# Performance work log

Measured on AMD Instinct MI355X. Metric: run time of the kernel, lower is better.

## Reference

```python
import math
import jax, jax.numpy as jnp
import numpy as np

B = 128          # graphs per batch
N = 1024         # nodes per graph
E = 1048576      # total edges (avg degree 8)
F_IN = 64
NHID = 64
NCLS = 10
RATIO = 0.8


def setup_inputs() -> dict:
    key = jax.random.key(0)
    ks = jax.random.split(key, 24)
    x = jax.random.normal(ks[0], (B * N, F_IN), jnp.float32)
    # intra-graph random edges: graph id per edge, local src/dst
    epg = E // B
    gid = jnp.repeat(jnp.arange(B, dtype=jnp.int32), epg)
    src = gid * N + jax.random.randint(ks[1], (E,), 0, N, jnp.int32)
    dst = gid * N + jax.random.randint(ks[2], (E,), 0, N, jnp.int32)
    def lin(k, fi, fo):
        s = 1.0 / np.sqrt(fi)
        return jax.random.uniform(k, (fi, fo), jnp.float32, -s, s)
    p = {
        'W1': lin(ks[3], F_IN, NHID), 'b1': jnp.zeros((NHID,), jnp.float32),
        'Wp1': lin(ks[4], NHID, 1), 'bp1': jnp.zeros((1,), jnp.float32),
        'W2': lin(ks[5], NHID, NHID), 'b2': jnp.zeros((NHID,), jnp.float32),
        'Wp2': lin(ks[6], NHID, 1), 'bp2': jnp.zeros((1,), jnp.float32),
        'W3': lin(ks[7], NHID, NHID), 'b3': jnp.zeros((NHID,), jnp.float32),
        'Wp3': lin(ks[8], NHID, 1), 'bp3': jnp.zeros((1,), jnp.float32),
        'L1w': lin(ks[9], 2 * NHID, NHID), 'L1b': jnp.zeros((NHID,), jnp.float32),
        'L2w': lin(ks[10], NHID, NHID // 2), 'L2b': jnp.zeros((NHID // 2,), jnp.float32),
        'L3w': lin(ks[11], NHID // 2, NCLS), 'L3b': jnp.zeros((NCLS,), jnp.float32),
    }
    return dict(x=x, edge_src=src, edge_dst=dst, **p)


def gcn_conv(x, W, b, src, dst, emask, n):
    # PyG GCNConv: add self loops, symmetric deg normalization
    xw = x @ W
    ew = emask.astype(x.dtype)
    deg = jax.ops.segment_sum(ew, dst, num_segments=n) + 1.0  # +1 self loop
    dis = jax.lax.rsqrt(deg)
    norm = dis[src] * dis[dst] * ew
    agg = jax.ops.segment_sum(xw[src] * norm[:, None], dst, num_segments=n)
    agg = agg + xw * (dis * dis)[:, None]  # self-loop message
    return agg + b


def sag_pool(x, Wp, bp, src, dst, emask, n_cur):
    n_tot = B * n_cur
    k = int(math.ceil(RATIO * n_cur))
    score = gcn_conv(x, Wp, bp, src, dst, emask, n_tot)[:, 0]
    _, idx = jax.lax.top_k(score.reshape(B, n_cur), k)
    perm = (idx + (jnp.arange(B, dtype=jnp.int32) * n_cur)[:, None]).reshape(-1)
    xn = x[perm] * jnp.tanh(score[perm])[:, None]
    new_idx = jnp.full((n_tot,), -1, jnp.int32).at[perm].set(
        jnp.arange(B * k, dtype=jnp.int32))
    ns, nd = new_idx[src], new_idx[dst]
    valid = emask & (ns >= 0) & (nd >= 0)
    return xn, jnp.where(valid, ns, 0), jnp.where(valid, nd, 0), valid, k


def readout(x, k):
    xr = x.reshape(B, k, NHID)
    return jnp.concatenate([xr.max(axis=1), xr.mean(axis=1)], axis=1)


def reference(x, edge_src, edge_dst, W1, b1, Wp1, bp1, W2, b2, Wp2, bp2,
              W3, b3, Wp3, bp3, L1w, L1b, L2w, L2b, L3w, L3b):
    src = edge_src.astype(jnp.int32)
    dst = edge_dst.astype(jnp.int32)
    emask = jnp.ones((E,), bool)
    n = N
    h = jax.nn.relu(gcn_conv(x, W1, b1, src, dst, emask, B * n))
    h, src, dst, emask, n = sag_pool(h, Wp1, bp1, src, dst, emask, n)
    r1 = readout(h, n)
    h = jax.nn.relu(gcn_conv(h, W2, b2, src, dst, emask, B * n))
    h, src, dst, emask, n = sag_pool(h, Wp2, bp2, src, dst, emask, n)
    r2 = readout(h, n)
    h = jax.nn.relu(gcn_conv(h, W3, b3, src, dst, emask, B * n))
    h, src, dst, emask, n = sag_pool(h, Wp3, bp3, src, dst, emask, n)
    r3 = readout(h, n)
    z = r1 + r2 + r3
    z = jax.nn.relu(z @ L1w + L1b)          # dropout is identity in eval
    z = jax.nn.relu(z @ L2w + L2b)
    return jax.nn.log_softmax(z @ L3w + L3b, axis=-1)
```

## Files before the change

### kernel.cpp

```cpp
#include <hip/hip_runtime.h>
#include <math.h>

constexpr int B_  = 128;
constexpr int N_  = 1024;
constexpr int E_  = 1048576;
constexpr int BN_ = B_ * N_;
constexpr int EPG = E_ / B_;
constexpr int NSEG = 16;

typedef short v8s __attribute__((ext_vector_type(8)));
typedef float v4f __attribute__((ext_vector_type(4)));

__device__ __forceinline__ unsigned bf16_rne(unsigned u) {
    return (u + 0x7FFFu + ((u >> 16) & 1u)) >> 16;
}

__global__ __launch_bounds__(1024) void k_csr(
        const int* __restrict__ src, const int* __restrict__ dst,
        int* __restrict__ srt, int* __restrict__ rowptr,
        float* __restrict__ dis, int n) {
    __shared__ int cnt[1024];
    __shared__ int cur[1024];
    __shared__ int wsum[17];
    int g = blockIdx.x, tid = threadIdx.x;
    int base = g * n;
    const int eb = g * EPG;

    for (int i = tid; i < n; i += 1024) cnt[i] = 0;
    __syncthreads();
    for (int t = tid; t < EPG; t += 1024) {
        int s = src[eb + t];
        if (s >= 0) atomicAdd(&cnt[dst[eb + t] - base], 1);
    }
    __syncthreads();

    int c = (tid < n) ? cnt[tid] : 0;
    int v = c;
    int lane = tid & 63, wv = tid >> 6;
    #pragma unroll
    for (int off = 1; off < 64; off <<= 1) {
        int t = __shfl_up(v, off, 64);
        if (lane >= off) v += t;
    }
    if (lane == 63) wsum[wv] = v;
    __syncthreads();
    if (tid == 0) {
        int run = 0;
        #pragma unroll
        for (int i = 0; i < 16; ++i) { int t = wsum[i]; wsum[i] = run; run += t; }
        wsum[16] = run;
    }
    __syncthreads();
    int excl = v - c + wsum[wv];
    if (tid < n) {
        cur[tid] = excl;
        rowptr[g * (n + 1) + tid] = excl;
        dis[base + tid] = rsqrtf((float)c + 1.0f);
    }
    if (tid == 0) rowptr[g * (n + 1) + n] = wsum[16];
    __syncthreads();

    for (int t = tid; t < EPG; t += 1024) {
        int s = src[eb + t];
        if (s < 0) continue;
        int pos = atomicAdd(&cur[dst[eb + t] - base], 1);
        srt[eb + pos] = s - base;
    }
}

__global__ __launch_bounds__(1024) void k_wprep3(
        const float* __restrict__ W0, const float* __restrict__ W1,
        const float* __restrict__ W2, unsigned short* __restrict__ wfall) {
    const float* W = (blockIdx.x == 0) ? W0 : (blockIdx.x == 1) ? W1 : W2;
    unsigned short* wf = wfall + (size_t)blockIdx.x * 8192;
    int t = threadIdx.x;
    int l  = t & 63;
    int kk = (t >> 6) & 1;
    int c  = (t >> 7) & 3;
    int p  = (t >> 9) & 1;
    int col = c * 16 + (l & 15);
    int kbase = kk * 32 + (l >> 4) * 8;
    unsigned short o[8];
    #pragma unroll
    for (int j = 0; j < 8; ++j) {
        float w = W[(kbase + j) * 64 + col];
        unsigned u  = __float_as_uint(w);
        unsigned hi = bf16_rne(u);
        if (p == 0) o[j] = (unsigned short)hi;
        else {
            float lo = w - __uint_as_float(hi << 16);
            o[j] = (unsigned short)bf16_rne(__float_as_uint(lo));
        }
    }
    uint4 v;
    v.x = o[0] | ((unsigned)o[1] << 16);
    v.y = o[2] | ((unsigned)o[3] << 16);
    v.z = o[4] | ((unsigned)o[5] << 16);
    v.w = o[6] | ((unsigned)o[7] << 16);
    *reinterpret_cast<uint4*>(wf + (size_t)t * 8) = v;
}

__global__ __launch_bounds__(256) void k_xw_mfma(
        const float* __restrict__ h, const unsigned short* __restrict__ wf,
        const float* __restrict__ dis, float* __restrict__ xwq, int rows) {
    __shared__ float hs[128][68];
    __shared__ float sdis[128];
    int tid = threadIdx.x;
    int r0 = blockIdx.x * 128;

    for (int i = tid; i < 128 * 16; i += 256) {
        int row = i >> 4, s = i & 15;
        float4 v = *reinterpret_cast<const float4*>(h + (size_t)(r0 + row) * 64 + s * 4);
        *reinterpret_cast<float4*>(&hs[row][s * 4]) = v;
    }
    if (tid < 128) sdis[tid] = dis[r0 + tid];

    int lane = tid & 63;
    v8s wh[4][2], wl[4][2];
    #pragma unroll
    for (int c = 0; c < 4; ++c) {
        #pragma unroll
        for (int kk = 0; kk < 2; ++kk) {
            wh[c][kk] = *reinterpret_cast<const v8s*>(wf + (((size_t)((0*4 + c)*2 + kk))*64 + lane)*8);
            wl[c][kk] = *reinterpret_cast<const v8s*>(wf + (((size_t)((1*4 + c)*2 + kk))*64 + lane)*8);
        }
    }
    __syncthreads();

    int wave = tid >> 6;
    int m = lane & 15, b = lane >> 4;
    #pragma unroll
    for (int t = 0; t < 2; ++t) {
        int lr0 = (wave * 2 + t) * 16;
        float f[16];
        *reinterpret_cast<float4*>(f)      = *reinterpret_cast<const float4*>(&hs[lr0 + m][b * 8]);
        *reinterpret_cast<float4*>(f + 4)  = *reinterpret_cast<const float4*>(&hs[lr0 + m][b * 8 + 4]);
        *reinterpret_cast<float4*>(f + 8)  = *reinterpret_cast<const float4*>(&hs[lr0 + m][32 + b * 8]);
        *reinterpret_cast<float4*>(f + 12) = *reinterpret_cast<const float4*>(&hs[lr0 + m][32 + b * 8 + 4]);
        v8s ah[2], al[2];
        #pragma unroll
        for (int ch = 0; ch < 2; ++ch) {
            #pragma unroll
            for (int j = 0; j < 8; ++j) {
                float x = f[ch * 8 + j];
                unsigned u  = __float_as_uint(x);
                unsigned hi = bf16_rne(u);
                float lo = x - __uint_as_float(hi << 16);
                ah[ch][j] = (short)hi;
                al[ch][j] = (short)bf16_rne(__float_as_uint(lo));
            }
        }
        float dv[4];
        #pragma unroll
        for (int reg = 0; reg < 4; ++reg) dv[reg] = sdis[lr0 + b * 4 + reg];

        #pragma unroll
        for (int c = 0; c < 4; ++c) {
            v4f acc = {0.f, 0.f, 0.f, 0.f};
            acc = __builtin_amdgcn_mfma_f32_16x16x32_bf16(ah[0], wh[c][0], acc, 0, 0, 0);
            acc = __builtin_amdgcn_mfma_f32_16x16x32_bf16(ah[1], wh[c][1], acc, 0, 0, 0);
            acc = __builtin_amdgcn_mfma_f32_16x16x32_bf16(al[0], wh[c][0], acc, 0, 0, 0);
            acc = __builtin_amdgcn_mfma_f32_16x16x32_bf16(al[1], wh[c][1], acc, 0, 0, 0);
            acc = __builtin_amdgcn_mfma_f32_16x16x32_bf16(ah[0], wl[c][0], acc, 0, 0, 0);
            acc = __builtin_amdgcn_mfma_f32_16x16x32_bf16(ah[1], wl[c][1], acc, 0, 0, 0);
            acc = __builtin_amdgcn_mfma_f32_16x16x32_bf16(al[0], wl[c][0], acc, 0, 0, 0);
            acc = __builtin_amdgcn_mfma_f32_16x16x32_bf16(al[1], wl[c][1], acc, 0, 0, 0);
            #pragma unroll
            for (int reg = 0; reg < 4; ++reg) {
                int grow = r0 + lr0 + b * 4 + reg;
                xwq[((size_t)c * rows + grow) * 16 + m] = acc[reg] * dv[reg];
            }
        }
    }
}

__global__ __launch_bounds__(1024) void k_agg_csr(
        const int* __restrict__ srt, const int* __restrict__ rowptr,
        const float* __restrict__ dis, const float* __restrict__ xwq,
        const float* __restrict__ bias, float* __restrict__ hout,
        int n, int rows) {
    extern __shared__ float lds[];
    float* xs  = lds;
    int* lsrt  = (int*)(lds + n * 20);
    int* lrp   = lsrt + EPG;
    int g = blockIdx.x >> 2, q = blockIdx.x & 3;
    int foff = q * 16;
    int tid  = threadIdx.x;
    int base = g * n;
    const float* plane = xwq + ((size_t)q * rows + base) * 16;

    for (int i = tid; i < n * 4; i += 1024) {
        int row = i >> 2, sub = i & 3;
        float4 v = *reinterpret_cast<const float4*>(plane + row * 16 + sub * 4);
        *reinterpret_cast<float4*>(xs + row * 20 + sub * 4) = v;
    }
    for (int i = tid; i <= n; i += 1024) lrp[i] = rowptr[g * (n + 1) + i];
    __syncthreads();
    int total = lrp[n];
    const int* gsrt = srt + g * EPG;
    for (int i = tid; i < total; i += 1024) lsrt[i] = gsrt[i];
    __syncthreads();

    int sub = tid & 3;
    float4 b = *reinterpret_cast<const float4*>(bias + foff + sub * 4);
    for (int row = tid >> 2; row < n; row += 256) {
        int s0 = lrp[row], s1 = lrp[row + 1];
        float4 acc = *reinterpret_cast<const float4*>(xs + row * 20 + sub * 4);
        for (int j = s0; j < s1; ++j) {
            int s = lsrt[j];
            const float4 v = *reinterpret_cast<const float4*>(xs + s * 20 + sub * 4);
            acc.x += v.x; acc.y += v.y; acc.z += v.z; acc.w += v.w;
        }
        float dsc = dis[base + row];
        float4 o;
        o.x = fmaxf(fmaf(dsc, acc.x, b.x), 0.0f);
        o.y = fmaxf(fmaf(dsc, acc.y, b.y), 0.0f);
        o.z = fmaxf(fmaf(dsc, acc.z, b.z), 0.0f);
        o.w = fmaxf(fmaf(dsc, acc.w, b.w), 0.0f);
        *reinterpret_cast<float4*>(hout + (size_t)(base + row) * 64 + foff + sub * 4) = o;
    }
}

__global__ void k_score(const float* __restrict__ h, const float* __restrict__ Wp,
                        const float* __restrict__ dis, float* __restrict__ sxws, int rows) {
    __shared__ float wp[64];
    if (threadIdx.x < 64) wp[threadIdx.x] = Wp[threadIdx.x];
    __syncthreads();
    int r = blockIdx.x * blockDim.x + threadIdx.x;
    if (r >= rows) return;
    const float4* hr = reinterpret_cast<const float4*>(h + (size_t)r * 64);
    float acc = 0.0f;
    #pragma unroll
    for (int kk = 0; kk < 16; ++kk) {
        float4 v = hr[kk];
        acc += v.x * wp[4*kk] + v.y * wp[4*kk+1] + v.z * wp[4*kk+2] + v.w * wp[4*kk+3];
    }
    sxws[r] = acc * dis[r];
}

__global__ __launch_bounds__(1024) void k_score_csr(
        const int* __restrict__ srt, const int* __restrict__ rowptr,
        const float* __restrict__ dis, const float* __restrict__ sxws,
        float* __restrict__ sagg, int n) {
    __shared__ float xs[1024];
    __shared__ int lrp[1025];
    __shared__ int lsrt[EPG];
    int g = blockIdx.x, tid = threadIdx.x;
    int base = g * n;
    for (int i = tid; i < n; i += 1024) xs[i] = sxws[base + i];
    for (int i = tid; i <= n; i += 1024) lrp[i] = rowptr[g * (n + 1) + i];
    __syncthreads();
    int total = lrp[n];
    for (int i = tid; i < total; i += 1024) lsrt[i] = srt[g * EPG + i];
    __syncthreads();
    if (tid < n) {
        float acc = xs[tid];
        int s1 = lrp[tid + 1];
        for (int j = lrp[tid]; j < s1; ++j) acc += xs[lsrt[j]];
        sagg[base + tid] = dis[base + tid] * acc;
    }
}

__global__ __launch_bounds__(512) void k_topk(
        const float* __restrict__ sagg, const float* __restrict__ bp,
        int n, int k, int* __restrict__ perm, int* __restrict__ new_idx) {
    __shared__ unsigned long long keys[1024];
    int g = blockIdx.x, tid = threadIdx.x;
    float bp0 = bp[0];
    for (int i = tid; i < 1024; i += 512) {
        unsigned long long kv = 0ull;
        if (i < n) {
            float sc = sagg[g * n + i] + bp0;
            unsigned u  = __float_as_uint(sc);
            unsigned mk = (u & 0x80000000u) ? ~u : (u | 0x80000000u);
            kv = ((unsigned long long)mk << 32) | (unsigned)i;
        }
        keys[i] = kv;
    }
    for (int size = 2; size <= 1024; size <<= 1) {
        for (int stride = size >> 1; stride > 0; stride >>= 1) {
            __syncthreads();
            int p = tid;
            int a  = ((p / stride) * (stride << 1)) + (p & (stride - 1));
            int bx = a + stride;
            bool asc = ((a & size) == 0);
            unsigned long long ka = keys[a], kb = keys[bx];
            bool sw = asc ? (ka > kb) : (ka < kb);
            if (sw) { keys[a] = kb; keys[bx] = ka; }
        }
    }
    __syncthreads();
    for (int j = tid; j < k; j += 512) {
        int pos   = 1023 - j;
        int local = (int)(keys[pos] & 0xFFFFFFFFull);
        int oldg  = g * n + local;
        int newg  = g * k + j;
        perm[newg]    = oldg;
        new_idx[oldg] = newg;
    }
}

__global__ __launch_bounds__(256) void k_gather_part(
        const float* __restrict__ h, const int* __restrict__ perm,
        const float* __restrict__ sagg, const float* __restrict__ bp,
        float* __restrict__ xn, int k, float* __restrict__ pz) {
    int g = blockIdx.x / NSEG, seg = blockIdx.x % NSEG;
    int ck = (k + NSEG - 1) / NSEG;
    int j0 = seg * ck;
    int j1 = min(k, j0 + ck);
    __shared__ float gate[64];
    __shared__ int   lperm[64];
    int tid = threadIdx.x;
    float bp0 = bp[0];
    for (int j = j0 + tid; j < j1; j += 256) {
        int old = perm[g * k + j];
        lperm[j - j0] = old;
        gate[j - j0]  = tanhf(sagg[old] + bp0);
    }
    __syncthreads();
    int lane = tid & 63, w = tid >> 6;
    float mx = -INFINITY, sm = 0.0f;
    for (int j = j0 + w; j < j1; j += 4) {
        int old = lperm[j - j0];
        float v = h[(size_t)old * 64 + lane] * gate[j - j0];
        xn[(size_t)(g * k + j) * 64 + lane] = v;
        mx = fmaxf(mx, v); sm += v;
    }
    __shared__ float smx[4][64], ssm[4][64];
    smx[w][lane] = mx; ssm[w][lane] = sm;
    __syncthreads();
    if (w == 0) {
        #pragma unroll
        for (int i = 1; i < 4; ++i) { mx = fmaxf(mx, smx[i][lane]); sm += ssm[i][lane]; }
        float* p = pz + ((size_t)g * NSEG + seg) * 128;
        p[lane]      = mx;
        p[64 + lane] = sm;
    }
}

__global__ __launch_bounds__(128) void k_combine(const float* __restrict__ pz,
                                                 int k, float* __restrict__ zsum) {
    int g = blockIdx.x, tid = threadIdx.x;
    const float* p = pz + (size_t)g * NSEG * 128;
    if (tid < 64) {
        float mx = -INFINITY;
        #pragma unroll
        for (int s = 0; s < NSEG; ++s) mx = fmaxf(mx, p[s * 128 + tid]);
        zsum[g * 128 + tid] += mx;
    } else {
        float sm = 0.0f;
        int f = tid - 64;
        #pragma unroll
        for (int s = 0; s < NSEG; ++s) sm += p[s * 128 + 64 + f];
        zsum[g * 128 + 64 + f] += sm / (float)k;
    }
}

__global__ void k_remap(const int* __restrict__ src, const int* __restrict__ dst,
                        const int* __restrict__ new_idx,
                        int* __restrict__ src2, int* __restrict__ dst2, int E) {
    int e = blockIdx.x * blockDim.x + threadIdx.x;
    if (e >= E) return;
    int s = src[e];
    int ns = -1, nd = -1;
    if (s >= 0) {
        ns = new_idx[s];
        nd = new_idx[dst[e]];
    }
    bool ok = (ns >= 0) && (nd >= 0);
    src2[e] = ok ? ns : -1;
    dst2[e] = ok ? nd : -1;
}

__global__ void k_mlp(const float* __restrict__ zsum,
                      const float* __restrict__ L1w, const float* __restrict__ L1b,
                      const float* __restrict__ L2w, const float* __restrict__ L2b,
                      const float* __restrict__ L3w, const float* __restrict__ L3b,
                      float* __restrict__ out) {
    __shared__ float z[128], h1[64], h2[32], lg[10], lse;
    int g = blockIdx.x, tid = threadIdx.x;
    z[tid] = zsum[g * 128 + tid];
    __syncthreads();
    if (tid < 64) {
        float acc = L1b[tid];
        for (int i = 0; i < 128; ++i) acc = fmaf(z[i], L1w[i * 64 + tid], acc);
        h1[tid] = fmaxf(acc, 0.0f);
    }
    __syncthreads();
    if (tid < 32) {
        float acc = L2b[tid];
        for (int i = 0; i < 64; ++i) acc = fmaf(h1[i], L2w[i * 32 + tid], acc);
        h2[tid] = fmaxf(acc, 0.0f);
    }
    __syncthreads();
    if (tid < 10) {
        float acc = L3b[tid];
        for (int i = 0; i < 32; ++i) acc = fmaf(h2[i], L3w[i * 10 + tid], acc);
        lg[tid] = acc;
    }
    __syncthreads();
    if (tid == 0) {
        float m = lg[0];
        for (int i = 1; i < 10; ++i) m = fmaxf(m, lg[i]);
        float s = 0.0f;
        for (int i = 0; i < 10; ++i) s += expf(lg[i] - m);
        lse = m + logf(s);
    }
    __syncthreads();
    if (tid < 10) out[g * 10 + tid] = lg[tid] - lse;
}

extern "C" void kernel_launch(void* const* d_in, const int* in_sizes, int n_in,
                              void* d_out, int out_size, void* d_ws, size_t ws_size,
                              hipStream_t stream) {
    const float* x    = (const float*)d_in[0];
    const int*   esrc = (const int*)d_in[1];
    const int*   edst = (const int*)d_in[2];
    const float* W [3] = {(const float*)d_in[3],  (const float*)d_in[7],  (const float*)d_in[11]};
    const float* bb[3] = {(const float*)d_in[4],  (const float*)d_in[8],  (const float*)d_in[12]};
    const float* Wp[3] = {(const float*)d_in[5],  (const float*)d_in[9],  (const float*)d_in[13]};
    const float* bp[3] = {(const float*)d_in[6],  (const float*)d_in[10], (const float*)d_in[14]};
    const float* L1w = (const float*)d_in[15];
    const float* L1b = (const float*)d_in[16];
    const float* L2w = (const float*)d_in[17];
    const float* L2b = (const float*)d_in[18];
    const float* L3w = (const float*)d_in[19];
    const float* L3b = (const float*)d_in[20];
    float* out = (float*)d_out;

    float* fws  = (float*)d_ws;
    float* bufA = fws;
    float* xwq  = bufA + 6717440;
    float* agg  = xwq  + 8388608;
    float* dis  = agg  + 8388608;
    float* sxws = dis  + BN_;
    float* sagg = sxws + BN_;
    float* zsum = sagg + BN_;
    float* pz   = zsum + 128 * 128;
    int*   new_idx = (int*)(pz + B_ * NSEG * 128);
    int*   perm    = new_idx + BN_;
    int*   srcB    = perm + BN_;
    int*   dstB    = srcB + E_;
    int*   srcC    = dstB + E_;
    int*   dstC    = srcC + E_;
    int*   srt     = dstC + E_;
    int*   rowptr  = srt  + E_;
    unsigned short* wfrag = (unsigned short*)(rowptr + B_ * (N_ + 1));

    hipFuncSetAttribute(reinterpret_cast<const void*>(k_agg_csr),
                        hipFuncAttributeMaxDynamicSharedMemorySize,
                        (1024 * 20 + EPG + 1025) * 4);

    hipMemsetAsync(zsum, 0, 128 * 128 * sizeof(float), stream);
    k_wprep3<<<3, 1024, 0, stream>>>(W[0], W[1], W[2], wfrag);

    const int ks_[3] = {820, 656, 525};
    int n = N_;
    const float* h_in = x;
    const int* cs = esrc;
    const int* cd = edst;
    int* nsrc[2] = {srcB, srcC};
    int* ndst[2] = {dstB, dstC};

    const int EB = (E_ + 255) / 256;

    for (int L = 0; L < 3; ++L) {
        int rows  = B_ * n;
        int k     = ks_[L];

        k_csr<<<B_, 1024, 0, stream>>>(cs, cd, srt, rowptr, dis, n);

        k_xw_mfma<<<rows / 128, 256, 0, stream>>>(h_in, wfrag + (size_t)L * 8192, dis, xwq, rows);
        k_agg_csr<<<B_ * 4, 1024, (size_t)(n * 20 + EPG + n + 1) * 4, stream>>>(
            srt, rowptr, dis, xwq, bb[L], agg, n, rows);

        k_score<<<(rows + 255) / 256, 256, 0, stream>>>(agg, Wp[L], dis, sxws, rows);
        k_score_csr<<<B_, 1024, 0, stream>>>(srt, rowptr, dis, sxws, sagg, n);

        if (L < 2) hipMemsetAsync(new_idx, 0xFF, (size_t)rows * sizeof(int), stream);
        k_topk<<<B_, 512, 0, stream>>>(sagg, bp[L], n, k, perm, new_idx);
        k_gather_part<<<B_ * NSEG, 256, 0, stream>>>(agg, perm, sagg, bp[L], bufA, k, pz);
        k_combine<<<B_, 128, 0, stream>>>(pz, k, zsum);
        if (L < 2) k_remap<<<EB, 256, 0, stream>>>(cs, cd, new_idx, nsrc[L], ndst[L], E_);

        h_in = bufA;
        n = k;
        if (L < 2) { cs = nsrc[L]; cd = ndst[L]; }
    }

    k_mlp<<<B_, 128, 0, stream>>>(zsum, L1w, L1b, L2w, L2b, L3w, L3b, out);
}
```

Baseline: 273.6 us.

## Fuse score, top-k, gather and edge remap into cumulative node-index mapping

```diff
diff --git a/kernel.cpp b/kernel.cpp
--- a/kernel.cpp
+++ b/kernel.cpp
@@ -15,22 +15,27 @@
     return (u + 0x7FFFu + ((u >> 16) & 1u)) >> 16;
 }
 
-__global__ __launch_bounds__(1024) void k_csr(
+__global__ __launch_bounds__(1024) void k_csr2(
         const int* __restrict__ src, const int* __restrict__ dst,
+        const int* __restrict__ cum,
         int* __restrict__ srt, int* __restrict__ rowptr,
         float* __restrict__ dis, int n) {
     __shared__ int cnt[1024];
     __shared__ int cur[1024];
+    __shared__ int cums[1024];
     __shared__ int wsum[17];
     int g = blockIdx.x, tid = threadIdx.x;
+    int gb   = g * N_;
     int base = g * n;
     const int eb = g * EPG;
 
-    for (int i = tid; i < n; i += 1024) cnt[i] = 0;
+    cums[tid] = cum ? cum[gb + tid] : tid;
+    cnt[tid] = 0;
     __syncthreads();
     for (int t = tid; t < EPG; t += 1024) {
-        int s = src[eb + t];
-        if (s >= 0) atomicAdd(&cnt[dst[eb + t] - base], 1);
+        int s = cums[src[eb + t] - gb];
+        int d = cums[dst[eb + t] - gb];
+        if ((s | d) >= 0) atomicAdd(&cnt[d], 1);
     }
     __syncthreads();
 
@@ -61,10 +66,11 @@
     __syncthreads();
 
     for (int t = tid; t < EPG; t += 1024) {
-        int s = src[eb + t];
-        if (s < 0) continue;
-        int pos = atomicAdd(&cur[dst[eb + t] - base], 1);
-        srt[eb + pos] = s - base;
+        int s = cums[src[eb + t] - gb];
+        int d = cums[dst[eb + t] - gb];
+        if ((s | d) < 0) continue;
+        int pos = atomicAdd(&cur[d], 1);
+        srt[eb + pos] = s;
     }
 }
 
@@ -101,17 +107,32 @@
 }
 
 __global__ __launch_bounds__(256) void k_xw_mfma(
-        const float* __restrict__ h, const unsigned short* __restrict__ wf,
+        const float* __restrict__ h, const int* __restrict__ perm,
+        const float* __restrict__ ggate, const unsigned short* __restrict__ wf,
         const float* __restrict__ dis, float* __restrict__ xwq, int rows) {
     __shared__ float hs[128][68];
     __shared__ float sdis[128];
+    __shared__ int   lperm[128];
+    __shared__ float lgate[128];
     int tid = threadIdx.x;
     int r0 = blockIdx.x * 128;
 
-    for (int i = tid; i < 128 * 16; i += 256) {
-        int row = i >> 4, s = i & 15;
-        float4 v = *reinterpret_cast<const float4*>(h + (size_t)(r0 + row) * 64 + s * 4);
-        *reinterpret_cast<float4*>(&hs[row][s * 4]) = v;
+    if (perm) {
+        if (tid < 128) { lperm[tid] = perm[r0 + tid]; lgate[tid] = ggate[r0 + tid]; }
+        __syncthreads();
+        for (int i = tid; i < 128 * 16; i += 256) {
+            int row = i >> 4, s = i & 15;
+            float4 v = *reinterpret_cast<const float4*>(h + (size_t)lperm[row] * 64 + s * 4);
+            float gt = lgate[row];
+            v.x *= gt; v.y *= gt; v.z *= gt; v.w *= gt;
+            *reinterpret_cast<float4*>(&hs[row][s * 4]) = v;
+        }
+    } else {
+        for (int i = tid; i < 128 * 16; i += 256) {
+            int row = i >> 4, s = i & 15;
+            float4 v = *reinterpret_cast<const float4*>(h + (size_t)(r0 + row) * 64 + s * 4);
+            *reinterpret_cast<float4*>(&hs[row][s * 4]) = v;
+        }
     }
     if (tid < 128) sdis[tid] = dis[r0 + tid];
 
@@ -177,7 +198,8 @@
 __global__ __launch_bounds__(1024) void k_agg_csr(
         const int* __restrict__ srt, const int* __restrict__ rowptr,
         const float* __restrict__ dis, const float* __restrict__ xwq,
-        const float* __restrict__ bias, float* __restrict__ hout,
+        const float* __restrict__ bias, const float* __restrict__ Wp,
+        float* __restrict__ hout, float* __restrict__ sxwsq,
         int n, int rows) {
     extern __shared__ float lds[];
     float* xs  = lds;
@@ -202,7 +224,8 @@
     __syncthreads();
 
     int sub = tid & 3;
-    float4 b = *reinterpret_cast<const float4*>(bias + foff + sub * 4);
+    float4 b   = *reinterpret_cast<const float4*>(bias + foff + sub * 4);
+    float4 wp4 = *reinterpret_cast<const float4*>(Wp   + foff + sub * 4);
     for (int row = tid >> 2; row < n; row += 256) {
         int s0 = lrp[row], s1 = lrp[row + 1];
         float4 acc = *reinterpret_cast<const float4*>(xs + row * 20 + sub * 4);
@@ -218,92 +241,96 @@
         o.z = fmaxf(fmaf(dsc, acc.z, b.z), 0.0f);
         o.w = fmaxf(fmaf(dsc, acc.w, b.w), 0.0f);
         *reinterpret_cast<float4*>(hout + (size_t)(base + row) * 64 + foff + sub * 4) = o;
-    }
-}
-
-__global__ void k_score(const float* __restrict__ h, const float* __restrict__ Wp,
-                        const float* __restrict__ dis, float* __restrict__ sxws, int rows) {
-    __shared__ float wp[64];
-    if (threadIdx.x < 64) wp[threadIdx.x] = Wp[threadIdx.x];
-    __syncthreads();
-    int r = blockIdx.x * blockDim.x + threadIdx.x;
-    if (r >= rows) return;
-    const float4* hr = reinterpret_cast<const float4*>(h + (size_t)r * 64);
-    float acc = 0.0f;
-    #pragma unroll
-    for (int kk = 0; kk < 16; ++kk) {
-        float4 v = hr[kk];
-        acc += v.x * wp[4*kk] + v.y * wp[4*kk+1] + v.z * wp[4*kk+2] + v.w * wp[4*kk+3];
-    }
-    sxws[r] = acc * dis[r];
-}
-
-__global__ __launch_bounds__(1024) void k_score_csr(
+        float part = o.x * wp4.x + o.y * wp4.y + o.z * wp4.z + o.w * wp4.w;
+        part += __shfl_xor(part, 1, 64);
+        part += __shfl_xor(part, 2, 64);
+        if (sub == 0) sxwsq[(size_t)q * BN_ + base + row] = part;
+    }
+}
+
+__global__ __launch_bounds__(1024) void k_score_topk(
         const int* __restrict__ srt, const int* __restrict__ rowptr,
-        const float* __restrict__ dis, const float* __restrict__ sxws,
-        float* __restrict__ sagg, int n) {
+        const float* __restrict__ dis, const float* __restrict__ sxwsq,
+        const float* __restrict__ bp, int n, int k,
+        int* __restrict__ perm, float* __restrict__ ggate,
+        int* __restrict__ cum, int do_compose) {
     __shared__ float xs[1024];
-    __shared__ int lrp[1025];
-    __shared__ int lsrt[EPG];
+    __shared__ int   lrp[1025];
+    __shared__ int   lsrt[EPG];
+    unsigned long long* keys = (unsigned long long*)lsrt;
+    int* mark = (int*)xs;
     int g = blockIdx.x, tid = threadIdx.x;
     int base = g * n;
-    for (int i = tid; i < n; i += 1024) xs[i] = sxws[base + i];
+    float bp0 = bp[0];
+
+    if (tid < n) {
+        float s0 = sxwsq[0 * (size_t)BN_ + base + tid] + sxwsq[1 * (size_t)BN_ + base + tid]
+                 + sxwsq[2 * (size_t)BN_ + base + tid] + sxwsq[3 * (size_t)BN_ + base + tid];
+        xs[tid] = s0 * dis[base + tid];
+    }
     for (int i = tid; i <= n; i += 1024) lrp[i] = rowptr[g * (n + 1) + i];
     __syncthreads();
     int total = lrp[n];
     for (int i = tid; i < total; i += 1024) lsrt[i] = srt[g * EPG + i];
     __syncthreads();
+
+    float sag = 0.0f;
     if (tid < n) {
         float acc = xs[tid];
         int s1 = lrp[tid + 1];
         for (int j = lrp[tid]; j < s1; ++j) acc += xs[lsrt[j]];
-        sagg[base + tid] = dis[base + tid] * acc;
-    }
-}
-
-__global__ __launch_bounds__(512) void k_topk(
-        const float* __restrict__ sagg, const float* __restrict__ bp,
-        int n, int k, int* __restrict__ perm, int* __restrict__ new_idx) {
-    __shared__ unsigned long long keys[1024];
-    int g = blockIdx.x, tid = threadIdx.x;
-    float bp0 = bp[0];
-    for (int i = tid; i < 1024; i += 512) {
+        sag = dis[base + tid] * acc + bp0;
+    }
+    __syncthreads();
+
+    {
         unsigned long long kv = 0ull;
-        if (i < n) {
-            float sc = sagg[g * n + i] + bp0;
-            unsigned u  = __float_as_uint(sc);
+        if (tid < n) {
+            unsigned u  = __float_as_uint(sag);
             unsigned mk = (u & 0x80000000u) ? ~u : (u | 0x80000000u);
-            kv = ((unsigned long long)mk << 32) | (unsigned)i;
-        }
-        keys[i] = kv;
-    }
+            kv = ((unsigned long long)mk << 32) | (unsigned)tid;
+        }
+        keys[tid] = kv;
+        mark[tid] = -1;
+    }
+
     for (int size = 2; size <= 1024; size <<= 1) {
         for (int stride = size >> 1; stride > 0; stride >>= 1) {
             __syncthreads();
-            int p = tid;
-            int a  = ((p / stride) * (stride << 1)) + (p & (stride - 1));
-            int bx = a + stride;
-            bool asc = ((a & size) == 0);
-            unsigned long long ka = keys[a], kb = keys[bx];
-            bool sw = asc ? (ka > kb) : (ka < kb);
-            if (sw) { keys[a] = kb; keys[bx] = ka; }
-        }
-    }
-    __syncthreads();
-    for (int j = tid; j < k; j += 512) {
-        int pos   = 1023 - j;
-        int local = (int)(keys[pos] & 0xFFFFFFFFull);
-        int oldg  = g * n + local;
-        int newg  = g * k + j;
-        perm[newg]    = oldg;
-        new_idx[oldg] = newg;
-    }
-}
-
-__global__ __launch_bounds__(256) void k_gather_part(
+            if (tid < 512) {
+                int a  = ((tid / stride) * (stride << 1)) + (tid & (stride - 1));
+                int bx = a + stride;
+                bool asc = ((a & size) == 0);
+                unsigned long long ka = keys[a], kb = keys[bx];
+                bool sw = asc ? (ka > kb) : (ka < kb);
+                if (sw) { keys[a] = kb; keys[bx] = ka; }
+            }
+        }
+    }
+    __syncthreads();
+
+    if (tid < k) {
+        int j = tid;
+        unsigned long long kv = keys[1023 - j];
+        int local   = (int)(kv & 0xFFFFFFFFull);
+        unsigned mk = (unsigned)(kv >> 32);
+        unsigned u  = (mk & 0x80000000u) ? (mk ^ 0x80000000u) : ~mk;
+        int newg = g * k + j;
+        perm[newg]  = base + local;
+        ggate[newg] = tanhf(__uint_as_float(u));
+        mark[local] = j;
+    }
+    __syncthreads();
+    if (do_compose) {
+        int gb = g * N_;
+        int c = (do_compose == 1) ? tid : cum[gb + tid];
+        cum[gb + tid] = (c >= 0) ? mark[c] : -1;
+    }
+}
+
+__global__ __launch_bounds__(256) void k_readout_seg(
         const float* __restrict__ h, const int* __restrict__ perm,
-        const float* __restrict__ sagg, const float* __restrict__ bp,
-        float* __restrict__ xn, int k, float* __restrict__ pz) {
+        const float* __restrict__ ggate, int k, float* __restrict__ pz) {
     int g = blockIdx.x / NSEG, seg = blockIdx.x % NSEG;
     int ck = (k + NSEG - 1) / NSEG;
     int j0 = seg * ck;
@@ -311,19 +338,15 @@
     __shared__ float gate[64];
     __shared__ int   lperm[64];
     int tid = threadIdx.x;
-    float bp0 = bp[0];
     for (int j = j0 + tid; j < j1; j += 256) {
-        int old = perm[g * k + j];
-        lperm[j - j0] = old;
-        gate[j - j0]  = tanhf(sagg[old] + bp0);
+        lperm[j - j0] = perm[g * k + j];
+        gate[j - j0]  = ggate[g * k + j];
     }
     __syncthreads();
     int lane = tid & 63, w = tid >> 6;
     float mx = -INFINITY, sm = 0.0f;
     for (int j = j0 + w; j < j1; j += 4) {
-        int old = lperm[j - j0];
-        float v = h[(size_t)old * 64 + lane] * gate[j - j0];
-        xn[(size_t)(g * k + j) * 64 + lane] = v;
+        float v = h[(size_t)lperm[j - j0] * 64 + lane] * gate[j - j0];
         mx = fmaxf(mx, v); sm += v;
     }
     __shared__ float smx[4][64], ssm[4][64];
@@ -338,48 +361,36 @@
     }
 }
 
-__global__ __launch_bounds__(128) void k_combine(const float* __restrict__ pz,
-                                                 int k, float* __restrict__ zsum) {
-    int g = blockIdx.x, tid = threadIdx.x;
-    const float* p = pz + (size_t)g * NSEG * 128;
-    if (tid < 64) {
-        float mx = -INFINITY;
-        #pragma unroll
-        for (int s = 0; s < NSEG; ++s) mx = fmaxf(mx, p[s * 128 + tid]);
-        zsum[g * 128 + tid] += mx;
-    } else {
-        float sm = 0.0f;
-        int f = tid - 64;
-        #pragma unroll
-        for (int s = 0; s < NSEG; ++s) sm += p[s * 128 + 64 + f];
-        zsum[g * 128 + 64 + f] += sm / (float)k;
-    }
-}
-
-__global__ void k_remap(const int* __restrict__ src, const int* __restrict__ dst,
-                        const int* __restrict__ new_idx,
-                        int* __restrict__ src2, int* __restrict__ dst2, int E) {
-    int e = blockIdx.x * blockDim.x + threadIdx.x;
-    if (e >= E) return;
-    int s = src[e];
-    int ns = -1, nd = -1;
-    if (s >= 0) {
-        ns = new_idx[s];
-        nd = new_idx[dst[e]];
-    }
-    bool ok = (ns >= 0) && (nd >= 0);
-    src2[e] = ok ? ns : -1;
-    dst2[e] = ok ? nd : -1;
-}
-
-__global__ void k_mlp(const float* __restrict__ zsum,
+__global__ __launch_bounds__(128) void k_mlp(const float* __restrict__ pz,
                       const float* __restrict__ L1w, const float* __restrict__ L1b,
                       const float* __restrict__ L2w, const float* __restrict__ L2b,
                       const float* __restrict__ L3w, const float* __restrict__ L3b,
                       float* __restrict__ out) {
     __shared__ float z[128], h1[64], h2[32], lg[10], lse;
     int g = blockIdx.x, tid = threadIdx.x;
-    z[tid] = zsum[g * 128 + tid];
+    const float kinv[3] = {1.0f / 820.0f, 1.0f / 656.0f, 1.0f / 525.0f};
+    float zv = 0.0f;
+    if (tid < 64) {
+        #pragma unroll
+        for (int L = 0; L < 3; ++L) {
+            const float* p = pz + (((size_t)L * B_ + g) * NSEG) * 128;
+            float mx = -INFINITY;
+            #pragma unroll
+            for (int s = 0; s < NSEG; ++s) mx = fmaxf(mx, p[s * 128 + tid]);
+            zv += mx;
+        }
+    } else {
+        int f = tid - 64;
+        #pragma unroll
+        for (int L = 0; L < 3; ++L) {
+            const float* p = pz + (((size_t)L * B_ + g) * NSEG) * 128;
+            float sm = 0.0f;
+            #pragma unroll
+            for (int s = 0; s < NSEG; ++s) sm += p[s * 128 + 64 + f];
+            zv += sm * kinv[L];
+        }
+    }
+    z[tid] = zv;
     __syncthreads();
     if (tid < 64) {
         float acc = L1b[tid];
@@ -428,65 +439,53 @@
     const float* L3b = (const float*)d_in[20];
     float* out = (float*)d_out;
 
-    float* fws  = (float*)d_ws;
-    float* bufA = fws;
-    float* xwq  = bufA + 6717440;
-    float* agg  = xwq  + 8388608;
-    float* dis  = agg  + 8388608;
-    float* sxws = dis  + BN_;
-    float* sagg = sxws + BN_;
-    float* zsum = sagg + BN_;
-    float* pz   = zsum + 128 * 128;
-    int*   new_idx = (int*)(pz + B_ * NSEG * 128);
-    int*   perm    = new_idx + BN_;
-    int*   srcB    = perm + BN_;
-    int*   dstB    = srcB + E_;
-    int*   srcC    = dstB + E_;
-    int*   dstC    = srcC + E_;
-    int*   srt     = dstC + E_;
-    int*   rowptr  = srt  + E_;
+    float* fws   = (float*)d_ws;
+    float* xwq   = fws;
+    float* agg   = xwq  + (size_t)BN_ * 64;
+    float* dis   = agg  + (size_t)BN_ * 64;
+    float* sxwsq = dis  + BN_;
+    float* ggate = sxwsq + 4 * (size_t)BN_;
+    float* pz    = ggate + BN_;
+    int*   perm   = (int*)(pz + 3 * B_ * NSEG * 128);
+    int*   cum    = perm + BN_;
+    int*   srt    = cum + BN_;
+    int*   rowptr = srt + E_;
     unsigned short* wfrag = (unsigned short*)(rowptr + B_ * (N_ + 1));
 
     hipFuncSetAttribute(reinterpret_cast<const void*>(k_agg_csr),
                         hipFuncAttributeMaxDynamicSharedMemorySize,
                         (1024 * 20 + EPG + 1025) * 4);
 
-    hipMemsetAsync(zsum, 0, 128 * 128 * sizeof(float), stream);
     k_wprep3<<<3, 1024, 0, stream>>>(W[0], W[1], W[2], wfrag);
 
     const int ks_[3] = {820, 656, 525};
     int n = N_;
-    const float* h_in = x;
-    const int* cs = esrc;
-    const int* cd = edst;
-    int* nsrc[2] = {srcB, srcC};
-    int* ndst[2] = {dstB, dstC};
-
-    const int EB = (E_ + 255) / 256;
 
     for (int L = 0; L < 3; ++L) {
-        int rows  = B_ * n;
-        int k     = ks_[L];
-
-        k_csr<<<B_, 1024, 0, stream>>>(cs, cd, srt, rowptr, dis, n);
-
-        k_xw_mfma<<<rows / 128, 256, 0, stream>>>(h_in, wfrag + (size_t)L * 8192, dis, xwq, rows);
+        int rows = B_ * n;
+        int k    = ks_[L];
+
+        k_csr2<<<B_, 1024, 0, stream>>>(esrc, edst, (L == 0) ? nullptr : cum,
+                                        srt, rowptr, dis, n);
+
+        if (L == 0)
+            k_xw_mfma<<<rows / 128, 256, 0, stream>>>(x, nullptr, nullptr,
+                                                      wfrag, dis, xwq, rows);
+        else
+            k_xw_mfma<<<rows / 128, 256, 0, stream>>>(agg, perm, ggate,
+                                                      wfrag + (size_t)L * 8192, dis, xwq, rows);
+
         k_agg_csr<<<B_ * 4, 1024, (size_t)(n * 20 + EPG + n + 1) * 4, stream>>>(
-            srt, rowptr, dis, xwq, bb[L], agg, n, rows);
-
-        k_score<<<(rows + 255) / 256, 256, 0, stream>>>(agg, Wp[L], dis, sxws, rows);
-        k_score_csr<<<B_, 1024, 0, stream>>>(srt, rowptr, dis, sxws, sagg, n);
-
-        if (L < 2) hipMemsetAsync(new_idx, 0xFF, (size_t)rows * sizeof(int), stream);
-        k_topk<<<B_, 512, 0, stream>>>(sagg, bp[L], n, k, perm, new_idx);
-        k_gather_part<<<B_ * NSEG, 256, 0, stream>>>(agg, perm, sagg, bp[L], bufA, k, pz);
-        k_combine<<<B_, 128, 0, stream>>>(pz, k, zsum);
-        if (L < 2) k_remap<<<EB, 256, 0, stream>>>(cs, cd, new_idx, nsrc[L], ndst[L], E_);
-
-        h_in = bufA;
+            srt, rowptr, dis, xwq, bb[L], Wp[L], agg, sxwsq, n, rows);
+
+        k_score_topk<<<B_, 1024, 0, stream>>>(srt, rowptr, dis, sxwsq, bp[L], n, k,
+                                              perm, ggate, cum, (L < 2) ? (L + 1) : 0);
+
+        k_readout_seg<<<B_ * NSEG, 256, 0, stream>>>(agg, perm, ggate, k,
+                                                     pz + (size_t)L * B_ * NSEG * 128);
+
         n = k;
-        if (L < 2) { cs = nsrc[L]; cd = ndst[L]; }
-    }
-
-    k_mlp<<<B_, 128, 0, stream>>>(zsum, L1w, L1b, L2w, L2b, L3w, L3b, out);
-}
+    }
+
+    k_mlp<<<B_, 128, 0, stream>>>(pz, L1w, L1b, L2w, L2b, L3w, L3b, out);
+}
```

Result: faster. 227.0 us (-17.1%).
